# Performance work log

Measured on AMD Instinct MI355X. Metric: run time of the kernel, lower is better.

## Reference

```python
import jax, jax.numpy as jnp
import numpy as np

SHAPES = ((100, 100), (50, 50), (25, 25), (13, 13))
D, NH, NP, NLVL, DFF, NLAYERS = 256, 8, 4, 4, 1024, 6
HD = D // NH
B = 2
Q = sum(h * w for h, w in SHAPES)
LEVEL_STARTS = np.cumsum([0] + [h * w for h, w in SHAPES])[:-1]


def _ref_points():
    # grid-center reference points, normalized to [0,1]; valid_ratios == 1 (masks all False)
    pts = []
    for (h, w) in SHAPES:
        ys = (np.arange(h) + 0.5) / h
        xs = (np.arange(w) + 0.5) / w
        gy, gx = np.meshgrid(ys, xs, indexing='ij')
        pts.append(np.stack([gx.ravel(), gy.ravel()], -1))
    return jnp.asarray(np.concatenate(pts, 0), jnp.float32)  # [Q,2] (x,y)


def layer_norm(x, g, b):
    m = x.mean(-1, keepdims=True)
    v = ((x - m) ** 2).mean(-1, keepdims=True)
    return (x - m) * jax.lax.rsqrt(v + 1e-5) * g + b


def bilinear_sample(val, lx, ly, H_, W_):
    # val [B,NH,HW,HD]; lx,ly [B,NH,Q,NP] in normalized [0,1] coords
    # matches F.grid_sample(align_corners=False, padding_mode='zeros')
    x = lx * W_ - 0.5
    y = ly * H_ - 0.5
    x0 = jnp.floor(x)
    y0 = jnp.floor(y)
    fx = x - x0
    fy = y - y0
    out = jnp.zeros(lx.shape + (HD,), val.dtype)
    for dy in (0, 1):
        for dx in (0, 1):
            xi = x0 + dx
            yi = y0 + dy
            w = (fx if dx else 1.0 - fx) * (fy if dy else 1.0 - fy)
            valid = (xi >= 0) & (xi < W_) & (yi >= 0) & (yi < H_)
            xi_c = jnp.clip(xi, 0, W_ - 1).astype(jnp.int32)
            yi_c = jnp.clip(yi, 0, H_ - 1).astype(jnp.int32)
            idx = (yi_c * W_ + xi_c).reshape(val.shape[0], NH, -1)  # [B,NH,Q*NP]
            g = jnp.take_along_axis(val, idx[..., None], axis=2).reshape(out.shape)
            out = out + (w * valid)[..., None] * g
    return out  # [B,NH,Q,NP,HD]


def ms_deform_attn(query, x, ref, Woff, boff, Wattn, battn, Wv, bv, Wo, bo):
    off = (query @ Woff + boff).reshape(B, Q, NH, NLVL, NP, 2)
    attn = jax.nn.softmax((query @ Wattn + battn).reshape(B, Q, NH, NLVL * NP), -1)
    attn = attn.reshape(B, Q, NH, NLVL, NP)
    val = (x @ Wv + bv).reshape(B, Q, NH, HD)
    norm = jnp.asarray([[w, h] for h, w in SHAPES], jnp.float32)  # offset_normalizer = (W,H)
    loc = ref[None, :, None, None, None, :] + off / norm[None, None, None, :, None, :]
    out = jnp.zeros((B, NH, Q, HD), x.dtype)
    for l, (h, w) in enumerate(SHAPES):
        s = int(LEVEL_STARTS[l])
        val_l = val[:, s:s + h * w].transpose(0, 2, 1, 3)  # [B,NH,HW,HD]
        lx = loc[:, :, :, l, :, 0].transpose(0, 2, 1, 3)   # [B,NH,Q,NP]
        ly = loc[:, :, :, l, :, 1].transpose(0, 2, 1, 3)
        sampled = bilinear_sample(val_l, lx, ly, h, w)     # [B,NH,Q,NP,HD]
        a = attn[:, :, :, l, :].transpose(0, 2, 1, 3)      # [B,NH,Q,NP]
        out = out + jnp.einsum('bhqp,bhqpd->bhqd', a, sampled)
    out = out.transpose(0, 2, 1, 3).reshape(B, Q, D)
    return out @ Wo + bo


def _forward(src0, src1, src2, src3, pos0, pos1, pos2, pos3, level_embed,
             Woff, boff, Wattn, battn, Wv, bv, Wo, bo,
             g1, b1, W1, bb1, W2, bb2, g2, b2):
    srcs = [src0, src1, src2, src3]
    poses = [pos0, pos1, pos2, pos3]
    src_flat = jnp.concatenate([s.reshape(B, D, -1).transpose(0, 2, 1) for s in srcs], 1)
    pos_flat = jnp.concatenate(
        [p.reshape(B, D, -1).transpose(0, 2, 1) + level_embed[i][None, None]
         for i, p in enumerate(poses)], 1)
    ref = _ref_points()
    x = src_flat
    for l in range(NLAYERS):
        q = x + pos_flat  # with_pos_embed
        x = x + ms_deform_attn(q, x, ref, Woff[l], boff[l], Wattn[l], battn[l],
                               Wv[l], bv[l], Wo[l], bo[l])
        x = layer_norm(x, g1[l], b1[l])
        ff = jax.nn.relu(x @ W1[l] + bb1[l]) @ W2[l] + bb2[l]
        x = layer_norm(x + ff, g2[l], b2[l])
    return x  # memory [B,Q,D]


def setup_inputs() -> dict:
    key = jax.random.key(0)
    ks = jax.random.split(key, 40)
    ctr = iter(range(40))

    def rn(shape, scale=1.0):
        return jax.random.normal(ks[next(ctr)], shape, jnp.float32) * scale

    d = {}
    for i, (h, w) in enumerate(SHAPES):
        d[f"src{i}"] = rn((B, D, h, w))
        d[f"pos{i}"] = rn((B, D, h, w))
    d["level_embed"] = rn((NLVL, D), 0.02)
    d["Woff"] = rn((NLAYERS, D, NH * NLVL * NP * 2), 0.01)
    d["boff"] = rn((NLAYERS, NH * NLVL * NP * 2), 0.1)
    d["Wattn"] = rn((NLAYERS, D, NH * NLVL * NP), 0.02)
    d["battn"] = jnp.zeros((NLAYERS, NH * NLVL * NP), jnp.float32)
    d["Wv"] = rn((NLAYERS, D, D), 0.02)
    d["bv"] = jnp.zeros((NLAYERS, D), jnp.float32)
    d["Wo"] = rn((NLAYERS, D, D), 0.02)
    d["bo"] = jnp.zeros((NLAYERS, D), jnp.float32)
    d["g1"] = jnp.ones((NLAYERS, D), jnp.float32)
    d["b1"] = jnp.zeros((NLAYERS, D), jnp.float32)
    d["W1"] = rn((NLAYERS, D, DFF), 0.02)
    d["bb1"] = jnp.zeros((NLAYERS, DFF), jnp.float32)
    d["W2"] = rn((NLAYERS, DFF, D), 0.02)
    d["bb2"] = jnp.zeros((NLAYERS, D), jnp.float32)
    d["g2"] = jnp.ones((NLAYERS, D), jnp.float32)
    d["b2"] = jnp.zeros((NLAYERS, D), jnp.float32)
    return d


def reference(src0, src1, src2, src3, pos0, pos1, pos2, pos3, level_embed,
              Woff, boff, Wattn, battn, Wv, bv, Wo, bo,
              g1, b1, W1, bb1, W2, bb2, g2, b2):
    return _forward(src0, src1, src2, src3, pos0, pos1, pos2, pos3, level_embed,
                    Woff, boff, Wattn, battn, Wv, bv, Wo, bo,
                    g1, b1, W1, bb1, W2, bb2, g2, b2)
```

## Files before the change

### kernel.cpp

```cpp
#include <hip/hip_runtime.h>
#include <hip/hip_fp16.h>
#include <math.h>

#define Q_ 13294
#define D_ 256
#define NLAYERS_ 6
#define MROWS 26588
#define MD ((size_t)MROWS * D_)

typedef unsigned short ushort_t;
typedef short bf16x8 __attribute__((ext_vector_type(8)));
typedef float f32x4 __attribute__((ext_vector_type(4)));
typedef ushort_t u16x8 __attribute__((ext_vector_type(8)));
typedef __fp16 fp16x2 __attribute__((ext_vector_type(2)));

__device__ __forceinline__ float u2f(ushort_t u) {
    return __uint_as_float(((unsigned)u) << 16);
}
__device__ __forceinline__ ushort_t f2bf(float f) {
    unsigned u = __float_as_uint(f);
    return (ushort_t)((u + 0x7fffu + ((u >> 16) & 1u)) >> 16);
}
__device__ __forceinline__ unsigned packh2(float a, float b) {
    fp16x2 t = __builtin_amdgcn_cvt_pkrtz(a, b);
    union { fp16x2 h; unsigned u; } c; c.h = t; return c.u;
}
__device__ __forceinline__ ushort_t f2h(float f) {
    _Float16 hv = (_Float16)f;
    union { _Float16 h; ushort_t u; } c; c.h = hv; return c.u;
}
__device__ __forceinline__ __half2 uash2(unsigned u) {
    union { unsigned u; __half2 h; } c; c.u = u; return c.h;
}
__device__ __forceinline__ void decode_row(int gr, int& b, int& l, int& p) {
    b = (gr >= Q_) ? 1 : 0;
    int q = gr - b * Q_;
    if (q < 10000)      { l = 0; p = q; }
    else if (q < 12500) { l = 1; p = q - 10000; }
    else if (q < 13125) { l = 2; p = q - 12500; }
    else                { l = 3; p = q - 13125; }
}

__global__ __launch_bounds__(256)
void flatten_kernel(const float* __restrict__ s0, const float* __restrict__ s1,
                    const float* __restrict__ s2, const float* __restrict__ s3,
                    const float* __restrict__ p0_, const float* __restrict__ p1_,
                    const float* __restrict__ p2_, const float* __restrict__ p3_,
                    const float* __restrict__ le,
                    float* __restrict__ X, ushort_t* __restrict__ Xb,
                    ushort_t* __restrict__ Tq)
{
    const int lHW[4] = {10000, 2500, 625, 169};
    const int lS[4]  = {0, 10000, 12500, 13125};
    int z = blockIdx.z;
    int l = z & 3, b = z >> 2;
    int HW = lHW[l];
    int p0 = blockIdx.x * 32;
    if (p0 >= HW) return;
    int d0 = blockIdx.y * 32;
    const float* src = (l == 0) ? s0 : (l == 1) ? s1 : (l == 2) ? s2 : s3;
    const float* pos = (l == 0) ? p0_ : (l == 1) ? p1_ : (l == 2) ? p2_ : p3_;
    int tx = threadIdx.x, ty = threadIdx.y;
    __shared__ float t[32][33];
    __shared__ float tp[32][33];
    #pragma unroll
    for (int i = 0; i < 4; ++i) {
        int d = d0 + ty + 8 * i, p = p0 + tx;
        size_t sidx = (size_t)(b * D_ + d) * HW + p;
        t[ty + 8 * i][tx] = (p < HW) ? src[sidx] : 0.f;
        if (Tq) tp[ty + 8 * i][tx] = (p < HW) ? pos[sidx] : 0.f;
    }
    __syncthreads();
    #pragma unroll
    for (int i = 0; i < 4; ++i) {
        int p = p0 + ty + 8 * i, d = d0 + tx;
        if (p < HW) {
            float v = t[tx][ty + 8 * i];
            size_t idx = (size_t)(b * Q_ + lS[l] + p) * D_ + d;
            X[idx] = v;
            Xb[idx] = f2bf(v);
            if (Tq)
                Tq[idx] = f2bf(v + tp[tx][ty + 8 * i] + le[l * D_ + d]);
        }
    }
}

__global__ __launch_bounds__(256)
void pl_kernel(const float* __restrict__ p0_, const float* __restrict__ p1_,
               const float* __restrict__ p2_, const float* __restrict__ p3_,
               const float* __restrict__ le, float* __restrict__ PL)
{
    const int lHW[4] = {10000, 2500, 625, 169};
    const int lS[4]  = {0, 10000, 12500, 13125};
    int z = blockIdx.z;
    int l = z & 3, b = z >> 2;
    int HW = lHW[l];
    int p0 = blockIdx.x * 32;
    if (p0 >= HW) return;
    int d0 = blockIdx.y * 32;
    const float* pos = (l == 0) ? p0_ : (l == 1) ? p1_ : (l == 2) ? p2_ : p3_;
    int tx = threadIdx.x, ty = threadIdx.y;
    __shared__ float t[32][33];
    #pragma unroll
    for (int i = 0; i < 4; ++i) {
        int d = d0 + ty + 8 * i, p = p0 + tx;
        t[ty + 8 * i][tx] = (p < HW) ? pos[(size_t)(b * D_ + d) * HW + p] : 0.f;
    }
    __syncthreads();
    #pragma unroll
    for (int i = 0; i < 4; ++i) {
        int p = p0 + ty + 8 * i, d = d0 + tx;
        if (p < HW)
            PL[(size_t)(b * Q_ + lS[l] + p) * D_ + d] =
                t[tx][ty + 8 * i] + le[l * D_ + d];
    }
}

__global__ __launch_bounds__(256)
void wconv_kernel(const float* __restrict__ Woff, const float* __restrict__ Wattn,
                  const float* __restrict__ Wv, const float* __restrict__ Wo,
                  const float* __restrict__ W1, const float* __restrict__ W2,
                  ushort_t* __restrict__ WBl)
{
    const int mk[6] = {256, 256, 256, 256, 256, 1024};
    const int mn[6] = {256, 128, 256, 256, 1024, 256};
    const int mo[6] = {0, 65536, 98304, 163840, 229376, 491520};
    int m = blockIdx.y;
    int K = mk[m], N = mn[m];
    int tilesN = N >> 5;
    int tiles = (K >> 5) * tilesN;
    int tid = blockIdx.x;
    if (tid >= tiles) return;
    int tk = tid / tilesN, tn = tid - tk * tilesN;
    const float* Wsrc = (m == 0) ? Woff : (m == 1) ? Wattn : (m == 2) ? Wv :
                        (m == 3) ? Wo : (m == 4) ? W1 : W2;
    ushort_t* dst = WBl + mo[m];
    __shared__ float t[32][33];
    int tx = threadIdx.x, ty = threadIdx.y;
    #pragma unroll
    for (int i = 0; i < 4; ++i) {
        int k = tk * 32 + ty + 8 * i, n = tn * 32 + tx;
        t[ty + 8 * i][tx] = Wsrc[(size_t)k * N + n];
    }
    __syncthreads();
    #pragma unroll
    for (int i = 0; i < 4; ++i) {
        int n = tn * 32 + ty + 8 * i, k = tk * 32 + tx;
        dst[(size_t)n * K + k] = f2bf(t[tx][ty + 8 * i]);
    }
}

__global__ __launch_bounds__(256)
void qmake_kernel(const float* __restrict__ X,
                  const float* __restrict__ p0_, const float* __restrict__ p1_,
                  const float* __restrict__ p2_, const float* __restrict__ p3_,
                  const float* __restrict__ le,
                  ushort_t* __restrict__ Tq, int row0, int mc)
{
    const int lHW[4] = {10000, 2500, 625, 169};
    int gid = blockIdx.x * 256 + threadIdx.x;
    int r = gid >> 6, d4 = gid & 63;
    if (r >= mc) return;
    int gr = row0 + r;
    int b, l, p;
    decode_row(gr, b, l, p);
    const float* pos = (l == 0) ? p0_ : (l == 1) ? p1_ : (l == 2) ? p2_ : p3_;
    int HW = lHW[l];
    int d = d4 * 4;
    float4 xv = *(const float4*)(X + (size_t)gr * D_ + d);
    ushort4 o;
    o.x = f2bf(xv.x + pos[(size_t)(b * D_ + d + 0) * HW + p] + le[l * D_ + d + 0]);
    o.y = f2bf(xv.y + pos[(size_t)(b * D_ + d + 1) * HW + p] + le[l * D_ + d + 1]);
    o.z = f2bf(xv.z + pos[(size_t)(b * D_ + d + 2) * HW + p] + le[l * D_ + d + 2]);
    o.w = f2bf(xv.w + pos[(size_t)(b * D_ + d + 3) * HW + p] + le[l * D_ + d + 3]);
    *(ushort4*)(Tq + (size_t)r * D_ + d) = o;
}

template<int BM, int CB>
__global__ __launch_bounds__(256)
void gemm_b(const ushort_t* __restrict__ A, const ushort_t* __restrict__ Wt,
            const float* __restrict__ bias, const float* __restrict__ bias2,
            int nsplit, const float* __restrict__ Rres,
            void* __restrict__ Cp, int M, int K, int ldc, int relu)
{
    constexpr int AI = BM / 32;
    constexpr int ES = (CB == 0) ? 4 : 2;
    constexpr size_t STAGE_B = (size_t)(BM + 128) * 64 * 2;
    constexpr size_t CT_B = (size_t)BM * 64 * ES;
    constexpr size_t LDS_B = (STAGE_B > CT_B) ? STAGE_B : CT_B;
    __shared__ __align__(16) char lds[LDS_B];
    ushort_t* As = (ushort_t*)lds;
    ushort_t* Bs = (ushort_t*)lds + (size_t)BM * 64;
    int t = threadIdx.x;

    int gx = gridDim.x, gy = gridDim.y;
    int nwg = gx * gy;
    int orig = blockIdx.y * gx + blockIdx.x;
    int qn = nwg >> 3, rn = nwg & 7;
    int xcd = orig & 7, idx = orig >> 3;
    int work = (xcd < rn ? xcd * (qn + 1) : rn * (qn + 1) + (xcd - rn) * qn) + idx;
    int bx = work / gy, by = work - bx * gy;
    int m0 = bx * BM, n0 = by * 128;

    int w = t >> 6, lane = t & 63;
    int wm = (w & 1) * (BM / 2), wn = (w >> 1) * 64;
    int lm = lane & 15, quad = lane >> 4;
    f32x4 acc[AI][4] = {};

    int srow = lane >> 3;
    int scol = (lane & 7) * 8;
    const ushort_t* Ab = A + (size_t)(m0 + w * (BM / 4) + srow) * K + scol;
    const ushort_t* Bb = Wt + (size_t)(n0 + w * 32 + srow) * K + scol;
    bool mfull = (m0 + BM <= M);

    for (int k0 = 0; k0 < K; k0 += 64) {
        if (mfull) {
            #pragma unroll
            for (int i = 0; i < AI; ++i)
                __builtin_amdgcn_global_load_lds(
                    (const void*)(Ab + (size_t)(i * 8) * K + k0),
                    (void*)&As[(w * (BM / 4) + i * 8) * 64], 16, 0, 0);
        } else {
            #pragma unroll
            for (int i = 0; i < AI; ++i)
                if (m0 + w * (BM / 4) + srow + i * 8 < M)
                    __builtin_amdgcn_global_load_lds(
                        (const void*)(Ab + (size_t)(i * 8) * K + k0),
                        (void*)&As[(w * (BM / 4) + i * 8) * 64], 16, 0, 0);
        }
        #pragma unroll
        for (int i = 0; i < 4; ++i)
            __builtin_amdgcn_global_load_lds(
                (const void*)(Bb + (size_t)(i * 8) * K + k0),
                (void*)&Bs[(w * 32 + i * 8) * 64], 16, 0, 0);
        __syncthreads();
        #pragma unroll
        for (int ks = 0; ks < 64; ks += 32) {
            bf16x8 af[AI], bfr[4];
            #pragma unroll
            for (int i = 0; i < AI; ++i)
                af[i] = *(const bf16x8*)&As[(wm + i * 16 + lm) * 64 + ks + quad * 8];
            #pragma unroll
            for (int j = 0; j < 4; ++j)
                bfr[j] = *(const bf16x8*)&Bs[(wn + j * 16 + lm) * 64 + ks + quad * 8];
            #pragma unroll
            for (int i = 0; i < AI; ++i)
                #pragma unroll
                for (int j = 0; j < 4; ++j)
                    acc[i][j] = __builtin_amdgcn_mfma_f32_16x16x32_bf16(
                        af[i], bfr[j], acc[i][j], 0, 0, 0);
        }
        __syncthreads();
    }

    constexpr int CHUNKS = (int)(CT_B / 16);
    constexpr int CPR = (64 * ES) / 16;
    constexpr int EPC = 16 / ES;
    int halfsel = w >> 1;
    #pragma unroll
    for (int half = 0; half < 2; ++half) {
        __syncthreads();
        if (halfsel == half) {
            #pragma unroll
            for (int i = 0; i < AI; ++i) {
                #pragma unroll
                for (int j = 0; j < 4; ++j) {
                    int col = j * 16 + lm;
                    int gcol = n0 + half * 64 + col;
                    float bc = (gcol < nsplit) ? bias[gcol] : bias2[gcol - nsplit];
                    #pragma unroll
                    for (int r = 0; r < 4; ++r) {
                        int rloc = wm + i * 16 + quad * 4 + r;
                        float v = acc[i][j][r] + bc;
                        if (relu) v = fmaxf(v, 0.f);
                        if (CB == 0) ((float*)lds)[rloc * 64 + col] = v;
                        else if (CB == 1) ((ushort_t*)lds)[rloc * 64 + col] = f2bf(v);
                        else ((ushort_t*)lds)[rloc * 64 + col] = f2h(v);
                    }
                }
            }
        }
        __syncthreads();
        for (int c0 = t; c0 < CHUNKS; c0 += 256) {
            int row = c0 / CPR, cp = c0 - row * CPR;
            int grow = m0 + row;
            if (grow >= M) continue;
            int gcol = n0 + half * 64 + cp * EPC;
            if (CB == 0) {
                float4 f = *(const float4*)(lds + (size_t)c0 * 16);
                if (Rres) {
                    float4 rr = *(const float4*)(Rres + (size_t)grow * ldc + gcol);
                    f.x += rr.x; f.y += rr.y; f.z += rr.z; f.w += rr.w;
                }
                *(float4*)((float*)Cp + (size_t)grow * ldc + gcol) = f;
            } else {
                uint4 val = *(const uint4*)(lds + (size_t)c0 * 16);
                *(uint4*)((ushort_t*)Cp + (size_t)grow * ldc + gcol) = val;
            }
        }
    }
}

__global__ __launch_bounds__(256)
void ln_kernel(const float* __restrict__ P, const float* __restrict__ g,
               const float* __restrict__ b, float* __restrict__ Xo,
               ushort_t* __restrict__ Xb,
               const float* __restrict__ PLf,
               const float* __restrict__ p0_, const float* __restrict__ p1_,
               const float* __restrict__ p2_, const float* __restrict__ p3_,
               const float* __restrict__ le, ushort_t* __restrict__ Tq,
               int row0, int mc)
{
    const int lHW[4] = {10000, 2500, 625, 169};
    int wave = threadIdx.x >> 6, lane = threadIdx.x & 63;
    int r = blockIdx.x * 4 + wave;
    if (r >= mc) return;
    const float* x = P + (size_t)r * D_;
    float4 v = *(const float4*)(x + lane * 4);
    float s = v.x + v.y + v.z + v.w;
    float sq = v.x * v.x + v.y * v.y + v.z * v.z + v.w * v.w;
    #pragma unroll
    for (int o = 32; o > 0; o >>= 1) {
        s += __shfl_xor(s, o, 64);
        sq += __shfl_xor(sq, o, 64);
    }
    float mean = s * (1.f / 256.f);
    float var = fmaxf(sq * (1.f / 256.f) - mean * mean, 0.f);
    float rs = rsqrtf(var + 1e-5f);
    float4 gv = *(const float4*)(g + lane * 4);
    float4 bv = *(const float4*)(b + lane * 4);
    float4 o;
    o.x = (v.x - mean) * rs * gv.x + bv.x;
    o.y = (v.y - mean) * rs * gv.y + bv.y;
    o.z = (v.z - mean) * rs * gv.z + bv.z;
    o.w = (v.w - mean) * rs * gv.w + bv.w;
    int gr = row0 + r;
    size_t base = (size_t)gr * D_ + lane * 4;
    *(float4*)(Xo + base) = o;
    ushort4 ob;
    ob.x = f2bf(o.x); ob.y = f2bf(o.y); ob.z = f2bf(o.z); ob.w = f2bf(o.w);
    *(ushort4*)(Xb + base) = ob;
    if (Tq) {
        ushort4 tq;
        if (PLf) {
            float4 pl = *(const float4*)(PLf + base);
            tq.x = f2bf(o.x + pl.x);
            tq.y = f2bf(o.y + pl.y);
            tq.z = f2bf(o.z + pl.z);
            tq.w = f2bf(o.w + pl.w);
        } else {
            int bb, l, p;
            decode_row(gr, bb, l, p);
            const float* pos = (l == 0) ? p0_ : (l == 1) ? p1_ : (l == 2) ? p2_ : p3_;
            int HW = lHW[l];
            int d = lane * 4;
            tq.x = f2bf(o.x + pos[(size_t)(bb * D_ + d + 0) * HW + p] + le[l * D_ + d + 0]);
            tq.y = f2bf(o.y + pos[(size_t)(bb * D_ + d + 1) * HW + p] + le[l * D_ + d + 1]);
            tq.z = f2bf(o.z + pos[(size_t)(bb * D_ + d + 2) * HW + p] + le[l * D_ + d + 2]);
            tq.w = f2bf(o.w + pos[(size_t)(bb * D_ + d + 3) * HW + p] + le[l * D_ + d + 3]);
        }
        *(ushort4*)(Tq + base) = tq;
    }
}

__global__ __launch_bounds__(256)
void sample_kernel(const ushort_t* __restrict__ LOG,
                   const ushort_t* __restrict__ VAL,
                   ushort_t* __restrict__ OUT, int row0, int mc)
{
    const int lW[4] = {100, 50, 25, 13};
    const int lS[4] = {0, 10000, 12500, 13125};
    const float invW[4] = {0.01f, 0.02f, 0.04f, 0.076923076923f};
    const unsigned mulM[4] = {5243u, 5243u, 5243u, 5042u};
    const int mulS[4] = {19, 18, 17, 16};

    __shared__ unsigned offs[8 * 8 * 68];
    __shared__ unsigned wts[8 * 8 * 36];

    int tid = threadIdx.x;

    int nb = gridDim.x, bid = blockIdx.x;
    int xcd = bid & 7, idx = bid >> 3;
    int qc = nb >> 3, rc = nb & 7;
    int swz = (xcd < rc ? xcd * (qc + 1) : rc * (qc + 1) + (xcd - rc) * qc) + idx;
    int brow0 = swz * 8;

    #pragma unroll
    for (int it = 0; it < 4; ++it) {
        int rr = it * 2 + (tid >> 7);
        int j  = tid & 127;
        int h  = j >> 4, pt = j & 15;
        int r  = brow0 + rr;
        bool ok = (r < mc);
        int gr = row0 + (ok ? r : 0);
        int b, lq, p;
        decode_row(gr, b, lq, p);
        unsigned prow = ((unsigned)p * mulM[lq]) >> mulS[lq];
        int pcol = p - (int)prow * lW[lq];
        float refx = (pcol + 0.5f) * invW[lq];
        float refy = ((float)prow + 0.5f) * invW[lq];

        const ushort_t* lg = LOG + (size_t)r * 384;
        float logit = ok ? u2f(lg[256 + h * 16 + pt]) : 0.f;
        float mx = logit;
        #pragma unroll
        for (int o = 8; o > 0; o >>= 1) mx = fmaxf(mx, __shfl_xor(mx, o, 16));
        float e = __expf(logit - mx);
        float ssum = e;
        #pragma unroll
        for (int o = 8; o > 0; o >>= 1) ssum += __shfl_xor(ssum, o, 16);
        float a = e / ssum;

        int l = pt >> 2;
        int Wl = lW[l];
        float ox = ok ? u2f(lg[h * 32 + pt * 2 + 0]) : 0.f;
        float oy = ok ? u2f(lg[h * 32 + pt * 2 + 1]) : 0.f;
        float xf = refx * (float)Wl + ox - 0.5f;
        float yf = refy * (float)Wl + oy - 0.5f;
        xf = fmaxf(fminf(xf, 1.0e6f), -1.0e6f);
        yf = fmaxf(fminf(yf, 1.0e6f), -1.0e6f);
        float x0f = floorf(xf), y0f = floorf(yf);
        float fx = xf - x0f, fy = yf - y0f;
        int x0 = (int)x0f, y0 = (int)y0f;
        int x1 = x0 + 1, y1 = y0 + 1;
        int x0c = min(max(x0, 0), Wl - 1), x1c = min(max(x1, 0), Wl - 1);
        int y0c = min(max(y0, 0), Wl - 1), y1c = min(max(y1, 0), Wl - 1);
        float vx0 = (x0 >= 0 && x0 < Wl) ? 1.f : 0.f;
        float vx1 = (x1 >= 0 && x1 < Wl) ? 1.f : 0.f;
        float vy0 = (y0 >= 0 && y0 < Wl) ? 1.f : 0.f;
        float vy1 = (y1 >= 0 && y1 < Wl) ? 1.f : 0.f;
        unsigned base_b = ((unsigned)(b * Q_ + lS[l]) * 256u + (unsigned)(h * 32)) * 2u;
        int di = (rr * 8 + h) * 68 + pt * 4;
        uint4 ov;
        ov.x = base_b + (unsigned)(y0c * Wl + x0c) * 512u;
        ov.y = base_b + (unsigned)(y0c * Wl + x1c) * 512u;
        ov.z = base_b + (unsigned)(y1c * Wl + x0c) * 512u;
        ov.w = base_b + (unsigned)(y1c * Wl + x1c) * 512u;
        *(uint4*)&offs[di] = ov;
        int dw = (rr * 8 + h) * 36 + pt * 2;
        uint2 wv;
        wv.x = packh2(a * (1.f - fx) * (1.f - fy) * vx0 * vy0,
                      a * fx * (1.f - fy) * vx1 * vy0);
        wv.y = packh2(a * (1.f - fx) * fy * vx0 * vy1,
                      a * fx * fy * vx1 * vy1);
        *(uint2*)&wts[dw] = wv;
    }
    __syncthreads();

    int r8 = tid >> 5;
    int r = brow0 + r8;
    if (r >= mc) return;
    int h = (tid >> 2) & 7;
    int cw = tid & 3;
    int dbase = (r8 * 8 + h) * 68;
    int dbw   = (r8 * 8 + h) * 36;
    const char* Vb = (const char*)VAL + cw * 16;

    __half2 a0 = __float2half2_rn(0.f), a1 = a0, a2 = a0, a3 = a0;
    #pragma unroll
    for (int g = 0; g < 8; ++g) {
        uint4 oA = *(const uint4*)&offs[dbase + g * 8 + 0];
        uint4 oB = *(const uint4*)&offs[dbase + g * 8 + 4];
        uint4 wp = *(const uint4*)&wts[dbw + g * 4];
        uint4 hv[8];
        hv[0] = *(const uint4*)(Vb + oA.x);
        hv[1] = *(const uint4*)(Vb + oA.y);
        hv[2] = *(const uint4*)(Vb + oA.z);
        hv[3] = *(const uint4*)(Vb + oA.w);
        hv[4] = *(const uint4*)(Vb + oB.x);
        hv[5] = *(const uint4*)(Vb + oB.y);
        hv[6] = *(const uint4*)(Vb + oB.z);
        hv[7] = *(const uint4*)(Vb + oB.w);
        __half2 w01 = uash2(wp.x), w23 = uash2(wp.y);
        __half2 w45 = uash2(wp.z), w67 = uash2(wp.w);
        __half2 we[8] = { __low2half2(w01), __high2half2(w01),
                          __low2half2(w23), __high2half2(w23),
                          __low2half2(w45), __high2half2(w45),
                          __low2half2(w67), __high2half2(w67) };
        #pragma unroll
        for (int jj = 0; jj < 8; ++jj) {
            a0 = __hfma2(uash2(hv[jj].x), we[jj], a0);
            a1 = __hfma2(uash2(hv[jj].y), we[jj], a1);
            a2 = __hfma2(uash2(hv[jj].z), we[jj], a2);
            a3 = __hfma2(uash2(hv[jj].w), we[jj], a3);
        }
    }
    float2 f0 = __half22float2(a0), f1 = __half22float2(a1);
    float2 f2v = __half22float2(a2), f3 = __half22float2(a3);
    u16x8 o;
    o[0] = f2bf(f0.x);  o[1] = f2bf(f0.y);
    o[2] = f2bf(f1.x);  o[3] = f2bf(f1.y);
    o[4] = f2bf(f2v.x); o[5] = f2bf(f2v.y);
    o[6] = f2bf(f3.x);  o[7] = f2bf(f3.y);
    *(u16x8*)(OUT + (size_t)r * D_ + h * 32 + cw * 8) = o;
}

extern "C" void kernel_launch(void* const* d_in, const int* in_sizes, int n_in,
                              void* d_out, int out_size, void* d_ws, size_t ws_size,
                              hipStream_t stream)
{
    bool interleaved = (in_sizes[0] == in_sizes[1]);
    int si[4], pi[4];
    for (int i = 0; i < 4; ++i) {
        si[i] = interleaved ? 2 * i : i;
        pi[i] = interleaved ? 2 * i + 1 : 4 + i;
    }
    const float* src0 = (const float*)d_in[si[0]];
    const float* src1 = (const float*)d_in[si[1]];
    const float* src2 = (const float*)d_in[si[2]];
    const float* src3 = (const float*)d_in[si[3]];
    const float* pos0 = (const float*)d_in[pi[0]];
    const float* pos1 = (const float*)d_in[pi[1]];
    const float* pos2 = (const float*)d_in[pi[2]];
    const float* pos3 = (const float*)d_in[pi[3]];
    const float* level_embed = (const float*)d_in[8];
    const float* Woff  = (const float*)d_in[9];
    const float* boff  = (const float*)d_in[10];
    const float* Wattn = (const float*)d_in[11];
    const float* battn = (const float*)d_in[12];
    const float* Wv = (const float*)d_in[13];
    const float* bv = (const float*)d_in[14];
    const float* Wo = (const float*)d_in[15];
    const float* bo = (const float*)d_in[16];
    const float* g1 = (const float*)d_in[17];
    const float* b1 = (const float*)d_in[18];
    const float* W1  = (const float*)d_in[19];
    const float* bb1 = (const float*)d_in[20];
    const float* W2  = (const float*)d_in[21];
    const float* bb2 = (const float*)d_in[22];
    const float* g2 = (const float*)d_in[23];
    const float* b2 = (const float*)d_in[24];

    ushort_t* VAL = (ushort_t*)d_in[si[0]];

    float* X = (float*)d_out;

    const int WV_T = 98304, WO_T = 163840, W1_T = 229376, W2_T = 491520;
    const size_t WB_ELEMS = 753664;

    const int cand[9] = {1, 2, 4, 8, 16, 32, 64, 128, 256};
    int NC = 256;
    for (int i = 0; i < 9; ++i) {
        int rc = (MROWS + cand[i] - 1) / cand[i];
        size_t need = WB_ELEMS * 2 + MD * 2 + (size_t)rc * 3072 + 1024;
        if (need <= ws_size) { NC = cand[i]; break; }
    }
    const int RC = (MROWS + NC - 1) / NC;
    const bool fused_tq = (NC == 1);
    const size_t base_need = WB_ELEMS * 2 + MD * 2 + (size_t)RC * 3072 + 1024;
    const bool use_pl = fused_tq && (base_need + MD * 4 <= ws_size);

    ushort_t* WBl  = (ushort_t*)d_ws;
    ushort_t* Xb   = (ushort_t*)((char*)d_ws + WB_ELEMS * 2);
    char* Rbase    = (char*)d_ws + WB_ELEMS * 2 + MD * 2;
    ushort_t* Tqu  = (ushort_t*)Rbase;
    ushort_t* LOGc = (ushort_t*)(Rbase + (size_t)RC * 512);
    float* PRE     = (float*)(Rbase + (size_t)RC * 2048);
    ushort_t* H1u  = (ushort_t*)Rbase;
    float* PLf     = use_pl ? (float*)(Rbase + (size_t)RC * 3072) : nullptr;

    flatten_kernel<<<dim3(313, 8, 8), dim3(32, 8), 0, stream>>>(
        src0, src1, src2, src3, pos0, pos1, pos2, pos3, level_embed,
        X, Xb, fused_tq ? Tqu : nullptr);
    if (use_pl)
        pl_kernel<<<dim3(313, 8, 8), dim3(32, 8), 0, stream>>>(
            pos0, pos1, pos2, pos3, level_embed, PLf);

    const int BIG = 1 << 30;

    for (int l = 0; l < NLAYERS_; ++l) {
        const float* Woff_l  = Woff  + (size_t)l * D_ * 256;
        const float* boff_l  = boff  + (size_t)l * 256;
        const float* Wattn_l = Wattn + (size_t)l * D_ * 128;
        const float* battn_l = battn + (size_t)l * 128;
        const float* Wv_l = Wv + (size_t)l * D_ * D_;
        const float* bv_l = bv + (size_t)l * D_;
        const float* Wo_l = Wo + (size_t)l * D_ * D_;
        const float* bo_l = bo + (size_t)l * D_;
        const float* g1_l = g1 + (size_t)l * D_;
        const float* b1_l = b1 + (size_t)l * D_;
        const float* W1_l  = W1  + (size_t)l * D_ * 1024;
        const float* bb1_l = bb1 + (size_t)l * 1024;
        const float* W2_l  = W2  + (size_t)l * 1024 * D_;
        const float* bb2_l = bb2 + (size_t)l * D_;
        const float* g2_l = g2 + (size_t)l * D_;
        const float* b2_l = b2 + (size_t)l * D_;

        wconv_kernel<<<dim3(256, 6), dim3(32, 8), 0, stream>>>(
            Woff_l, Wattn_l, Wv_l, Wo_l, W1_l, W2_l, WBl);

        gemm_b<64, 2><<<dim3((MROWS + 63) / 64, 2), 256, 0, stream>>>(
            Xb, WBl + WV_T, bv_l, nullptr, BIG, nullptr, VAL, MROWS, 256, 256, 0);

        for (int c = 0; c < NC; ++c) {
            int row0 = c * RC;
            int mc = MROWS - row0; if (mc > RC) mc = RC;
            if (mc <= 0) break;
            if (!fused_tq)
                qmake_kernel<<<(mc * 64 + 255) / 256, 256, 0, stream>>>(
                    X, pos0, pos1, pos2, pos3, level_embed, Tqu, row0, mc);
            gemm_b<64, 1><<<dim3((mc + 63) / 64, 3), 256, 0, stream>>>(
                Tqu, WBl, boff_l, battn_l, 256, nullptr, LOGc, mc, 256, 384, 0);
            sample_kernel<<<(mc + 7) / 8, 256, 0, stream>>>(
                LOGc, VAL, Tqu, row0, mc);
            gemm_b<64, 0><<<dim3((mc + 63) / 64, 2), 256, 0, stream>>>(
                Tqu, WBl + WO_T, bo_l, nullptr, BIG,
                X + (size_t)row0 * D_, PRE, mc, 256, 256, 0);
            ln_kernel<<<(mc + 3) / 4, 256, 0, stream>>>(
                PRE, g1_l, b1_l, X, Xb, nullptr,
                pos0, pos1, pos2, pos3, level_embed, (ushort_t*)nullptr,
                row0, mc);
        }

        for (int c = 0; c < NC; ++c) {
            int row0 = c * RC;
            int mc = MROWS - row0; if (mc > RC) mc = RC;
            if (mc <= 0) break;
            float* Xc = X + (size_t)row0 * D_;
            gemm_b<128, 1><<<dim3((mc + 127) / 128, 8), 256, 0, stream>>>(
                Xb + (size_t)row0 * D_, WBl + W1_T, bb1_l, nullptr, BIG,
                nullptr, H1u, mc, 256, 1024, 1);
            gemm_b<64, 0><<<dim3((mc + 63) / 64, 2), 256, 0, stream>>>(
                H1u, WBl + W2_T, bb2_l, nullptr, BIG, Xc, PRE, mc, 1024, 256, 0);
            ushort_t* TqNext = (fused_tq && l < NLAYERS_ - 1) ? Tqu : nullptr;
            ln_kernel<<<(mc + 3) / 4, 256, 0, stream>>>(
                PRE, g2_l, b2_l, X, Xb, PLf,
                pos0, pos1, pos2, pos3, level_embed, TqNext,
                row0, mc);
        }
    }
}
```

Baseline: 1.307 ms.

## Fuse output-projection and FFN-down GEMMs with residual add and LayerNorm

Adds a gemm_ln kernel that computes a 32-row by 256-column GEMM tile, adds bias and residual, then reduces row statistics across waves in LDS and writes the normalized fp32 and bf16 outputs. When the workspace allows full fusion it is used for both the Wo and W2 projections, and the W2 path also writes the next layer's query tensor into a separate buffer. This removes the fp32 PRE round-trip and the separate LayerNorm launches. In exchange each block must cover all 256 output columns, which means fewer blocks and a single-buffered K loop, and X is read as the residual while being written in place.

```diff
diff --git a/kernel.cpp b/kernel.cpp
--- a/kernel.cpp
+++ b/kernel.cpp
@@ -297,6 +297,158 @@
                 uint4 val = *(const uint4*)(lds + (size_t)c0 * 16);
                 *(uint4*)((ushort_t*)Cp + (size_t)grow * ldc + gcol) = val;
             }
+        }
+    }
+}
+
+__global__ __launch_bounds__(256)
+void gemm_ln(const ushort_t* __restrict__ A, const ushort_t* __restrict__ Wt,
+             const float* __restrict__ bias, const float* __restrict__ Rres,
+             const float* __restrict__ g, const float* __restrict__ b,
+             float* __restrict__ Xo, ushort_t* __restrict__ Xb,
+             const float* __restrict__ PLf, ushort_t* __restrict__ Tq,
+             int M, int K)
+{
+    __shared__ __align__(16) char lds[36864];
+    ushort_t* As = (ushort_t*)lds;
+    ushort_t* Bs = (ushort_t*)(lds + 4096);
+    float* Ct   = (float*)lds;
+    float* psum = (float*)(lds + 33280);
+    float* mrs  = (float*)(lds + 34304);
+
+    int t = threadIdx.x;
+    int nwg = gridDim.x, orig = blockIdx.x;
+    int qn = nwg >> 3, rn = nwg & 7;
+    int xcd = orig & 7, idx = orig >> 3;
+    int work = (xcd < rn ? xcd * (qn + 1) : rn * (qn + 1) + (xcd - rn) * qn) + idx;
+    int m0 = work * 32;
+
+    int w = t >> 6, lane = t & 63;
+    int lm = lane & 15, quad = lane >> 4;
+    int colbase = w * 64;
+    f32x4 acc[2][4] = {};
+
+    int srow = lane >> 3;
+    int scol = (lane & 7) * 8;
+    const ushort_t* Ab = A + (size_t)(m0 + w * 8 + srow) * K + scol;
+    const ushort_t* Bb = Wt + (size_t)(colbase + srow) * K + scol;
+    bool mfull = (m0 + 32 <= M);
+
+    for (int k0 = 0; k0 < K; k0 += 64) {
+        if (mfull) {
+            __builtin_amdgcn_global_load_lds((const void*)(Ab + k0),
+                (void*)&As[(w * 8) * 64], 16, 0, 0);
+        } else {
+            if (m0 + w * 8 + srow < M)
+                __builtin_amdgcn_global_load_lds((const void*)(Ab + k0),
+                    (void*)&As[(w * 8) * 64], 16, 0, 0);
+        }
+        #pragma unroll
+        for (int i = 0; i < 8; ++i)
+            __builtin_amdgcn_global_load_lds(
+                (const void*)(Bb + (size_t)(i * 8) * K + k0),
+                (void*)&Bs[(colbase + i * 8) * 64], 16, 0, 0);
+        __syncthreads();
+        #pragma unroll
+        for (int ks = 0; ks < 64; ks += 32) {
+            bf16x8 af[2], bfr[4];
+            #pragma unroll
+            for (int i = 0; i < 2; ++i)
+                af[i] = *(const bf16x8*)&As[(i * 16 + lm) * 64 + ks + quad * 8];
+            #pragma unroll
+            for (int j = 0; j < 4; ++j)
+                bfr[j] = *(const bf16x8*)&Bs[(colbase + j * 16 + lm) * 64 + ks + quad * 8];
+            #pragma unroll
+            for (int i = 0; i < 2; ++i)
+                #pragma unroll
+                for (int j = 0; j < 4; ++j)
+                    acc[i][j] = __builtin_amdgcn_mfma_f32_16x16x32_bf16(
+                        af[i], bfr[j], acc[i][j], 0, 0, 0);
+        }
+        __syncthreads();
+    }
+
+    float bcol[4];
+    #pragma unroll
+    for (int j = 0; j < 4; ++j) bcol[j] = bias[colbase + j * 16 + lm];
+    #pragma unroll
+    for (int i = 0; i < 2; ++i) {
+        #pragma unroll
+        for (int r = 0; r < 4; ++r) {
+            int grow = m0 + i * 16 + quad * 4 + r;
+            bool ok = grow < M;
+            #pragma unroll
+            for (int j = 0; j < 4; ++j) {
+                float res = ok ? Rres[(size_t)grow * 256 + colbase + j * 16 + lm] : 0.f;
+                acc[i][j][r] += bcol[j] + res;
+            }
+        }
+    }
+    #pragma unroll
+    for (int i = 0; i < 2; ++i) {
+        #pragma unroll
+        for (int r = 0; r < 4; ++r) {
+            float s = acc[i][0][r] + acc[i][1][r] + acc[i][2][r] + acc[i][3][r];
+            float q = acc[i][0][r] * acc[i][0][r] + acc[i][1][r] * acc[i][1][r]
+                    + acc[i][2][r] * acc[i][2][r] + acc[i][3][r] * acc[i][3][r];
+            #pragma unroll
+            for (int m = 1; m <= 8; m <<= 1) {
+                s += __shfl_xor(s, m, 64);
+                q += __shfl_xor(q, m, 64);
+            }
+            if (lm == 0) {
+                int row = i * 16 + quad * 4 + r;
+                psum[(w * 32 + row) * 2 + 0] = s;
+                psum[(w * 32 + row) * 2 + 1] = q;
+            }
+        }
+    }
+    __syncthreads();
+    if (t < 32) {
+        float s = psum[t * 2] + psum[(32 + t) * 2] + psum[(64 + t) * 2] + psum[(96 + t) * 2];
+        float q = psum[t * 2 + 1] + psum[(32 + t) * 2 + 1]
+                + psum[(64 + t) * 2 + 1] + psum[(96 + t) * 2 + 1];
+        float mean = s * (1.f / 256.f);
+        float var = fmaxf(q * (1.f / 256.f) - mean * mean, 0.f);
+        mrs[t * 2 + 0] = mean;
+        mrs[t * 2 + 1] = rsqrtf(var + 1e-5f);
+    }
+    __syncthreads();
+    float gc[4], bc2[4];
+    #pragma unroll
+    for (int j = 0; j < 4; ++j) {
+        gc[j]  = g[colbase + j * 16 + lm];
+        bc2[j] = b[colbase + j * 16 + lm];
+    }
+    #pragma unroll
+    for (int i = 0; i < 2; ++i) {
+        #pragma unroll
+        for (int r = 0; r < 4; ++r) {
+            int row = i * 16 + quad * 4 + r;
+            float mean = mrs[row * 2], rs = mrs[row * 2 + 1];
+            #pragma unroll
+            for (int j = 0; j < 4; ++j)
+                Ct[row * 260 + colbase + j * 16 + lm] =
+                    (acc[i][j][r] - mean) * rs * gc[j] + bc2[j];
+        }
+    }
+    __syncthreads();
+    for (int c0 = t; c0 < 32 * 64; c0 += 256) {
+        int row = c0 >> 6, cp = c0 & 63;
+        int grow = m0 + row;
+        if (grow >= M) continue;
+        float4 f = *(const float4*)&Ct[row * 260 + cp * 4];
+        size_t gbase = (size_t)grow * 256 + cp * 4;
+        *(float4*)(Xo + gbase) = f;
+        ushort4 ob;
+        ob.x = f2bf(f.x); ob.y = f2bf(f.y); ob.z = f2bf(f.z); ob.w = f2bf(f.w);
+        *(ushort4*)(Xb + gbase) = ob;
+        if (Tq) {
+            float4 pl = *(const float4*)(PLf + gbase);
+            ushort4 tq;
+            tq.x = f2bf(f.x + pl.x); tq.y = f2bf(f.y + pl.y);
+            tq.z = f2bf(f.z + pl.z); tq.w = f2bf(f.w + pl.w);
+            *(ushort4*)(Tq + gbase) = tq;
         }
     }
 }
@@ -549,6 +701,7 @@
     const bool fused_tq = (NC == 1);
     const size_t base_need = WB_ELEMS * 2 + MD * 2 + (size_t)RC * 3072 + 1024;
     const bool use_pl = fused_tq && (base_need + MD * 4 <= ws_size);
+    const bool full_fuse = use_pl;
 
     ushort_t* WBl  = (ushort_t*)d_ws;
     ushort_t* Xb   = (ushort_t*)((char*)d_ws + WB_ELEMS * 2);
@@ -557,6 +710,7 @@
     ushort_t* LOGc = (ushort_t*)(Rbase + (size_t)RC * 512);
     float* PRE     = (float*)(Rbase + (size_t)RC * 2048);
     ushort_t* H1u  = (ushort_t*)Rbase;
+    ushort_t* Tq2  = (ushort_t*)(Rbase + (size_t)RC * 2048);
     float* PLf     = use_pl ? (float*)(Rbase + (size_t)RC * 3072) : nullptr;
 
     flatten_kernel<<<dim3(313, 8, 8), dim3(32, 8), 0, stream>>>(
@@ -567,6 +721,7 @@
             pos0, pos1, pos2, pos3, level_embed, PLf);
 
     const int BIG = 1 << 30;
+    const int GLN = (MROWS + 31) / 32;
 
     for (int l = 0; l < NLAYERS_; ++l) {
         const float* Woff_l  = Woff  + (size_t)l * D_ * 256;
@@ -599,17 +754,24 @@
             if (!fused_tq)
                 qmake_kernel<<<(mc * 64 + 255) / 256, 256, 0, stream>>>(
                     X, pos0, pos1, pos2, pos3, level_embed, Tqu, row0, mc);
+            const ushort_t* Qcur = (full_fuse && l > 0) ? Tq2 : Tqu;
             gemm_b<64, 1><<<dim3((mc + 63) / 64, 3), 256, 0, stream>>>(
-                Tqu, WBl, boff_l, battn_l, 256, nullptr, LOGc, mc, 256, 384, 0);
+                Qcur, WBl, boff_l, battn_l, 256, nullptr, LOGc, mc, 256, 384, 0);
             sample_kernel<<<(mc + 7) / 8, 256, 0, stream>>>(
                 LOGc, VAL, Tqu, row0, mc);
-            gemm_b<64, 0><<<dim3((mc + 63) / 64, 2), 256, 0, stream>>>(
-                Tqu, WBl + WO_T, bo_l, nullptr, BIG,
-                X + (size_t)row0 * D_, PRE, mc, 256, 256, 0);
-            ln_kernel<<<(mc + 3) / 4, 256, 0, stream>>>(
-                PRE, g1_l, b1_l, X, Xb, nullptr,
-                pos0, pos1, pos2, pos3, level_embed, (ushort_t*)nullptr,
-                row0, mc);
+            if (full_fuse) {
+                gemm_ln<<<GLN, 256, 0, stream>>>(
+                    Tqu, WBl + WO_T, bo_l, X, g1_l, b1_l, X, Xb,
+                    nullptr, nullptr, MROWS, 256);
+            } else {
+                gemm_b<64, 0><<<dim3((mc + 63) / 64, 2), 256, 0, stream>>>(
+                    Tqu, WBl + WO_T, bo_l, nullptr, BIG,
+                    X + (size_t)row0 * D_, PRE, mc, 256, 256, 0);
+                ln_kernel<<<(mc + 3) / 4, 256, 0, stream>>>(
+                    PRE, g1_l, b1_l, X, Xb, nullptr,
+                    pos0, pos1, pos2, pos3, level_embed, (ushort_t*)nullptr,
+                    row0, mc);
+            }
         }
 
         for (int c = 0; c < NC; ++c) {
@@ -620,13 +782,20 @@
             gemm_b<128, 1><<<dim3((mc + 127) / 128, 8), 256, 0, stream>>>(
                 Xb + (size_t)row0 * D_, WBl + W1_T, bb1_l, nullptr, BIG,
                 nullptr, H1u, mc, 256, 1024, 1);
-            gemm_b<64, 0><<<dim3((mc + 63) / 64, 2), 256, 0, stream>>>(
-                H1u, WBl + W2_T, bb2_l, nullptr, BIG, Xc, PRE, mc, 1024, 256, 0);
-            ushort_t* TqNext = (fused_tq && l < NLAYERS_ - 1) ? Tqu : nullptr;
-            ln_kernel<<<(mc + 3) / 4, 256, 0, stream>>>(
-                PRE, g2_l, b2_l, X, Xb, PLf,
-                pos0, pos1, pos2, pos3, level_embed, TqNext,
-                row0, mc);
-        }
-    }
-}
+            if (full_fuse) {
+                ushort_t* TqNext = (l < NLAYERS_ - 1) ? Tq2 : nullptr;
+                gemm_ln<<<GLN, 256, 0, stream>>>(
+                    H1u, WBl + W2_T, bb2_l, X, g2_l, b2_l, X, Xb,
+                    PLf, TqNext, MROWS, 1024);
+            } else {
+                gemm_b<64, 0><<<dim3((mc + 63) / 64, 2), 256, 0, stream>>>(
+                    H1u, WBl + W2_T, bb2_l, nullptr, BIG, Xc, PRE, mc, 1024, 256, 0);
+                ushort_t* TqNext = (fused_tq && l < NLAYERS_ - 1) ? Tqu : nullptr;
+                ln_kernel<<<(mc + 3) / 4, 256, 0, stream>>>(
+                    PRE, g2_l, b2_l, X, Xb, PLf,
+                    pos0, pos1, pos2, pos3, level_embed, TqNext,
+                    row0, mc);
+            }
+        }
+    }
+}
```

Measured after the change: 1.209 ms. -7.5%, faster.
